# Kernel optimization log

Hardware: AMD Instinct MI355X
Metric: run time of the kernel (lower is better)

Reference implementation:

```python
import jax, jax.numpy as jnp
import numpy as np

N_EMBD = 1024
N_HEAD = 16
LATENT = 64
HEAD_DIM = N_EMBD // N_HEAD
B, T = 2, 2048
SCALE = 1.0 / np.sqrt(LATENT)


def setup_inputs() -> dict:
    key = jax.random.key(0)
    ks = jax.random.split(key, 10)
    s = lambda fan_in: 1.0 / np.sqrt(fan_in)
    return {
        "x": jax.random.normal(ks[0], (B, T, N_EMBD), dtype=jnp.float32),
        "Wq": jax.random.normal(ks[1], (N_EMBD, N_EMBD), dtype=jnp.float32) * s(N_EMBD),
        "bq": jnp.zeros((N_EMBD,), dtype=jnp.float32),
        "Wk": jax.random.normal(ks[2], (N_EMBD, N_HEAD * LATENT), dtype=jnp.float32) * s(N_EMBD),
        "bk": jnp.zeros((N_HEAD * LATENT,), dtype=jnp.float32),
        "Wv": jax.random.normal(ks[3], (N_EMBD, N_HEAD * LATENT), dtype=jnp.float32) * s(N_EMBD),
        "bv": jnp.zeros((N_HEAD * LATENT,), dtype=jnp.float32),
        "Wo": jax.random.normal(ks[4], (N_HEAD * LATENT, N_EMBD), dtype=jnp.float32) * s(N_HEAD * LATENT),
        "bo": jnp.zeros((N_EMBD,), dtype=jnp.float32),
        "Wc": jax.random.normal(ks[5], (HEAD_DIM, LATENT), dtype=jnp.float32) * s(HEAD_DIM),
    }


def reference(x, Wq, bq, Wk, bk, Wv, bv, Wo, bo, Wc):
    Bv, Tv, C = x.shape
    # projections
    q = (x @ Wq + bq).reshape(Bv, Tv, N_HEAD, HEAD_DIM)        # [B,T,H,Dh]
    k = (x @ Wk + bk).reshape(Bv, Tv, N_HEAD, LATENT)          # [B,T,H,L]
    v = (x @ Wv + bv).reshape(Bv, Tv, N_HEAD, LATENT)          # [B,T,H,L]
    # compress q into latent dim: [B,T,H,L]
    qc = jnp.einsum("bthd,dl->bthl", q, Wc)
    # attention scores [B,H,T,T]
    att = jnp.einsum("bthl,bshl->bhts", qc, k) * SCALE
    causal = jnp.tril(jnp.ones((Tv, Tv), dtype=bool))
    att = jnp.where(causal[None, None], att, -jnp.inf)
    att = jax.nn.softmax(att, axis=-1)
    y = jnp.einsum("bhts,bshl->bthl", att, v).reshape(Bv, Tv, N_HEAD * LATENT)
    return y @ Wo + bo
```

## Files before the change

kernel.cpp:

```cpp
#include <hip/hip_runtime.h>
#include <stdint.h>

#define TT 2048
#define BB 2
#define MROWS (BB*TT)
#define LSCALE 0.18033688011112043f

typedef unsigned short u16;
typedef __bf16 bf16x8 __attribute__((ext_vector_type(8)));
typedef float f32x4 __attribute__((ext_vector_type(4)));
typedef short s16x8 __attribute__((ext_vector_type(8)));
typedef unsigned short u16x4 __attribute__((ext_vector_type(4)));

#define GLOBAL_AS const __attribute__((address_space(1))) void*
#define LDS_AS __attribute__((address_space(3))) void*

__device__ __forceinline__ u16 f2b(float f){
  uint32_t u = __builtin_bit_cast(uint32_t, f);
  u = (u + 0x7FFFu + ((u >> 16) & 1u)) >> 16;
  return (u16)u;
}

__global__ __launch_bounds__(256) void prep(
    const float* __restrict__ x, const float* __restrict__ Wq,
    const float* __restrict__ Wc, const float* __restrict__ bq,
    const float* __restrict__ Wk, const float* __restrict__ Wv,
    const float* __restrict__ Wo,
    u16* __restrict__ xb, u16* __restrict__ WqcT, u16* __restrict__ WkT,
    u16* __restrict__ WvT, u16* __restrict__ WoT, float* __restrict__ bqc){
  const int i = blockIdx.x, t = threadIdx.x;
  if (i < 4096){
    int id = i * 256 + t;
    float4 v = ((const float4*)x)[id];
    u16x4 o; o.x = f2b(v.x); o.y = f2b(v.y); o.z = f2b(v.z); o.w = f2b(v.w);
    ((u16x4*)xb)[id] = o;
    return;
  }
  if (i < 7168){
    int j = i - 4096;
    int z = j >> 10, rem = j & 1023;
    const float* in = (z == 0) ? Wk : (z == 1) ? Wv : Wo;
    u16* out = (z == 0) ? WkT : (z == 1) ? WvT : WoT;
    __shared__ float tl[32][33];
    int tx = t & 31, ty = t >> 5;
    int c0 = (rem & 31) * 32, r0 = (rem >> 5) * 32;
    #pragma unroll
    for (int k = 0; k < 32; k += 8)
      tl[ty + k][tx] = in[(size_t)(r0 + ty + k) * 1024 + c0 + tx];
    __syncthreads();
    #pragma unroll
    for (int k = 0; k < 32; k += 8)
      out[(size_t)(c0 + ty + k) * 1024 + r0 + tx] = f2b(tl[tx][ty + k]);
    return;
  }
  __shared__ float wc[4096];
  #pragma unroll
  for (int k = 0; k < 16; ++k) wc[k * 256 + t] = Wc[k * 256 + t];
  __syncthreads();
  if (i == 7424){
    #pragma unroll
    for (int k = 0; k < 4; ++k){
      int nn = t * 4 + k;
      int h = nn >> 6, lc = nn & 63;
      float a = 0.f;
      #pragma unroll
      for (int dd = 0; dd < 64; ++dd) a += bq[h * 64 + dd] * wc[dd * 64 + lc];
      bqc[nn] = a;
    }
    return;
  }
  __shared__ float tile[64][65];
  const int j = i - 7168;
  const int db = j >> 4, hb = j & 15;
  {
    int dl = t >> 2, lq = t & 3;
    const float4* wq4 = (const float4*)(Wq + (size_t)(db * 64 + dl) * 1024 + hb * 64);
    float wqr[64];
    #pragma unroll
    for (int k = 0; k < 16; ++k){
      float4 v = wq4[k];
      wqr[k * 4] = v.x; wqr[k * 4 + 1] = v.y; wqr[k * 4 + 2] = v.z; wqr[k * 4 + 3] = v.w;
    }
    #pragma unroll
    for (int jj = 0; jj < 16; ++jj){
      int lc = lq * 16 + jj;
      float a = 0.f;
      #pragma unroll
      for (int dd = 0; dd < 64; ++dd) a += wqr[dd] * wc[dd * 64 + lc];
      tile[dl][lc] = a;
    }
  }
  __syncthreads();
  {
    int nl = t >> 2, dq = t & 3;
    u16* dst = WqcT + (size_t)(hb * 64 + nl) * 1024 + db * 64 + dq * 16;
    #pragma unroll
    for (int k = 0; k < 16; ++k)
      dst[k] = f2b(tile[dq * 16 + k][nl]);
  }
}

__global__ void transpose_v(const u16* __restrict__ vb, u16* __restrict__ vt){
  __shared__ u16 t[32][34];
  int tx = threadIdx.x & 31, ty = threadIdx.x >> 5;
  int s0 = blockIdx.x * 32, d0 = blockIdx.y * 32, bh = blockIdx.z;
  int b = bh >> 4, h = bh & 15;
  #pragma unroll
  for (int i = 0; i < 32; i += 8)
    t[ty + i][tx] = vb[(size_t)(b * TT + s0 + ty + i) * 1024 + h * 64 + d0 + tx];
  __syncthreads();
  #pragma unroll
  for (int i = 0; i < 32; i += 8)
    vt[((size_t)bh * 64 + d0 + ty + i) * TT + s0 + tx] = t[tx][ty + i];
}

__device__ __forceinline__ void gemm_tile(const u16* __restrict__ A, const u16* __restrict__ BT,
                                          int m0, int n0, int K, f32x4 (&acc)[4][4],
                                          u16* As, u16* Bs, int tid){
  const int wv = tid >> 6, l = tid & 63;
  const int aoff = ((wv >> 1) * 64 + (l & 15)) * 32 + ((l >> 4) << 3);
  const int boff = ((wv & 1) * 64 + (l & 15)) * 32 + ((l >> 4) << 3);
  const int ob0 = wv * 1024 + l * 16;
  for (int kt = 0; kt < K; kt += 32){
    __syncthreads();
    #pragma unroll
    for (int j = 0; j < 2; ++j){
      int ob = ob0 + j * 4096;
      int row = ob >> 6, col = (ob & 63) >> 1;
      __builtin_amdgcn_global_load_lds((GLOBAL_AS)(A + (size_t)(m0 + row) * 1024 + kt + col),
                                       (LDS_AS)(As + wv * 512 + j * 2048), 16, 0, 0);
      __builtin_amdgcn_global_load_lds((GLOBAL_AS)(BT + (size_t)(n0 + row) * 1024 + kt + col),
                                       (LDS_AS)(Bs + wv * 512 + j * 2048), 16, 0, 0);
    }
    __syncthreads();
    bf16x8 av[4], bw[4];
    #pragma unroll
    for (int m = 0; m < 4; ++m) av[m] = *(const bf16x8*)(As + aoff + m * 512);
    #pragma unroll
    for (int n = 0; n < 4; ++n) bw[n] = *(const bf16x8*)(Bs + boff + n * 512);
    #pragma unroll
    for (int m = 0; m < 4; ++m)
      #pragma unroll
      for (int n = 0; n < 4; ++n)
        acc[m][n] = __builtin_amdgcn_mfma_f32_16x16x32_bf16(av[m], bw[n], acc[m][n], 0, 0, 0);
  }
}

__global__ __launch_bounds__(256) void gemm_qkv(
    const u16* __restrict__ xb,
    const u16* __restrict__ W0T, const u16* __restrict__ W1T, const u16* __restrict__ W2T,
    const float* __restrict__ b0, const float* __restrict__ b1, const float* __restrict__ b2,
    u16* __restrict__ o0, u16* __restrict__ o1, u16* __restrict__ o2){
  __shared__ u16 As[4096], Bs[4096];
  const int z = blockIdx.z;
  const u16* BT = (z == 0) ? W0T : (z == 1) ? W1T : W2T;
  const float* bias = (z == 0) ? b0 : (z == 1) ? b1 : b2;
  u16* Out = (z == 0) ? o0 : (z == 1) ? o1 : o2;
  const float osc = (z == 0) ? LSCALE : 1.0f;
  const int n0 = blockIdx.x * 128, m0 = blockIdx.y * 128;
  const int tid = threadIdx.x, wv = tid >> 6, l = tid & 63;
  f32x4 acc[4][4] = {};
  gemm_tile(xb, BT, m0, n0, 1024, acc, As, Bs, tid);
  const int wr = wv >> 1, wc = wv & 1;
  #pragma unroll
  for (int n = 0; n < 4; ++n){
    int col = n0 + wc * 64 + n * 16 + (l & 15);
    float bb = bias[col];
    #pragma unroll
    for (int m = 0; m < 4; ++m){
      int r0 = m0 + wr * 64 + m * 16 + ((l >> 4) << 2);
      #pragma unroll
      for (int r = 0; r < 4; ++r)
        Out[(size_t)(r0 + r) * 1024 + col] = f2b((acc[m][n][r] + bb) * osc);
    }
  }
}

__global__ __launch_bounds__(256) void gemm_o(
    const u16* __restrict__ A, const u16* __restrict__ BT,
    const float* __restrict__ bias, float* __restrict__ Out){
  __shared__ u16 As[2048], Bs[4096];
  const int n0 = blockIdx.x * 128, m0 = blockIdx.y * 64;
  const int tid = threadIdx.x, wv = tid >> 6, l = tid & 63;
  const int wr = wv >> 1, wc = wv & 1;
  const int aoff = (wr * 32 + (l & 15)) * 32 + ((l >> 4) << 3);
  const int boff = (wc * 64 + (l & 15)) * 32 + ((l >> 4) << 3);
  const int obA = wv * 1024 + l * 16;
  const int rowA = obA >> 6, colA = (obA & 63) >> 1;
  const int ob0 = wv * 1024 + l * 16;
  f32x4 acc[2][4] = {};
  for (int kt = 0; kt < 1024; kt += 32){
    __syncthreads();
    __builtin_amdgcn_global_load_lds((GLOBAL_AS)(A + (size_t)(m0 + rowA) * 1024 + kt + colA),
                                     (LDS_AS)(As + wv * 512), 16, 0, 0);
    #pragma unroll
    for (int j = 0; j < 2; ++j){
      int ob = ob0 + j * 4096;
      int row = ob >> 6, col = (ob & 63) >> 1;
      __builtin_amdgcn_global_load_lds((GLOBAL_AS)(BT + (size_t)(n0 + row) * 1024 + kt + col),
                                       (LDS_AS)(Bs + wv * 512 + j * 2048), 16, 0, 0);
    }
    __syncthreads();
    bf16x8 av[2], bw[4];
    #pragma unroll
    for (int m = 0; m < 2; ++m) av[m] = *(const bf16x8*)(As + aoff + m * 512);
    #pragma unroll
    for (int n = 0; n < 4; ++n) bw[n] = *(const bf16x8*)(Bs + boff + n * 512);
    #pragma unroll
    for (int m = 0; m < 2; ++m)
      #pragma unroll
      for (int n = 0; n < 4; ++n)
        acc[m][n] = __builtin_amdgcn_mfma_f32_16x16x32_bf16(av[m], bw[n], acc[m][n], 0, 0, 0);
  }
  #pragma unroll
  for (int n = 0; n < 4; ++n){
    int col = n0 + wc * 64 + n * 16 + (l & 15);
    float bb = bias[col];
    #pragma unroll
    for (int m = 0; m < 2; ++m){
      int r0 = m0 + wr * 32 + m * 16 + ((l >> 4) << 2);
      #pragma unroll
      for (int r = 0; r < 4; ++r)
        Out[(size_t)(r0 + r) * 1024 + col] = acc[m][n][r] + bb;
    }
  }
}

__device__ const uint8_t qtab[32] = {
  31, 30, 29, 28, 27, 26, 25, 24,
   0,  1,  2,  3,  4,  5,  6,  7,
  23, 22, 21, 20, 19, 18, 17, 16,
   8,  9, 10, 11, 12, 13, 14, 15
};

__global__ __launch_bounds__(256) void attn(
    const u16* __restrict__ qcg, const u16* __restrict__ kg,
    const u16* __restrict__ vtg, u16* __restrict__ yg){
  __shared__ u16 Ks[4096], Vs[4096];
  __shared__ u16 Ps[4096];
  const int idx = blockIdx.x;
  const int qt = qtab[idx >> 5], bh = idx & 31;
  const int b = bh >> 4, h = bh & 15;
  const int q0 = qt * 64;
  const int tid = threadIdx.x, wv = tid >> 6, l = tid & 63;
  const int c4 = l >> 4, q16 = l & 15;
  const size_t base = (size_t)b * TT * 1024 + h * 64;
  const u16* Q = qcg + base;
  const u16* K = kg + base;
  const u16* Vt = vtg + (size_t)bh * 64 * TT;

  const int sr = tid >> 3;
  const int sc = (tid & 7) ^ (sr & 7);
  const u16* gK = K + (size_t)sr * 1024 + sc * 8;
  const u16* gV = Vt + (size_t)sr * TT + sc * 8;

  bf16x8 qf[2];
  {
    int qr = q0 + wv * 16 + q16;
    #pragma unroll
    for (int ks = 0; ks < 2; ++ks)
      qf[ks] = *(const bf16x8*)(Q + (size_t)qr * 1024 + ks * 32 + (c4 << 3));
  }
  bf16x8 ones;
  {
    s16x8 o1;
    #pragma unroll
    for (int j = 0; j < 8; ++j) o1[j] = (short)0x3F80;
    ones = __builtin_bit_cast(bf16x8, o1);
  }
  f32x4 yacc[4] = {};
  f32x4 sacc = {};
  float mrow = -1e30f;

  uint32_t* const PsW = (uint32_t*)Ps + wv * 512 + q16 * 32;
  const int pm = (q16 & 7) << 2;

  u16* const kd = Ks + wv * 512;
  u16* const vd = Vs + wv * 512;

  const int nt = qt + 1;
  for (int st = 0; st < nt; ++st){
    {
      const size_t o = (size_t)st * 64;
      __builtin_amdgcn_global_load_lds((GLOBAL_AS)(gK + o * 1024), (LDS_AS)kd, 16, 0, 0);
      __builtin_amdgcn_global_load_lds((GLOBAL_AS)(gK + (o + 32) * 1024), (LDS_AS)(kd + 2048), 16, 0, 0);
      __builtin_amdgcn_global_load_lds((GLOBAL_AS)(gV + o), (LDS_AS)vd, 16, 0, 0);
      __builtin_amdgcn_global_load_lds((GLOBAL_AS)(gV + o + 32 * TT), (LDS_AS)(vd + 2048), 16, 0, 0);
    }
    asm volatile("s_waitcnt vmcnt(0)" ::: "memory");
    __builtin_amdgcn_sched_barrier(0);
    __builtin_amdgcn_s_barrier();
    __builtin_amdgcn_sched_barrier(0);
    const int s0 = st * 64;
    f32x4 sf[4] = {};
    __builtin_amdgcn_s_setprio(1);
    #pragma unroll
    for (int ks = 0; ks < 2; ++ks)
      #pragma unroll
      for (int nf = 0; nf < 4; ++nf){
        int r = nf * 16 + q16, c = ks * 4 + c4;
        bf16x8 kf = *(const bf16x8*)(Ks + (r * 8 + (c ^ (r & 7))) * 8);
        sf[nf] = __builtin_amdgcn_mfma_f32_16x16x32_bf16(kf, qf[ks], sf[nf], 0, 0, 0);
      }
    __builtin_amdgcn_s_setprio(0);
    const int qa = q0 + wv * 16 + q16;
    float p[4][4];
    const bool domask = (st == qt);
    #pragma unroll
    for (int nf = 0; nf < 4; ++nf)
      #pragma unroll
      for (int r = 0; r < 4; ++r){
        float v_ = sf[nf][r];
        if (domask && (s0 + nf * 16 + c4 * 4 + r > qa)) v_ = -1e30f;
        p[nf][r] = v_;
      }
    float tmax = fmaxf(fmaxf(p[0][0], p[0][1]), p[0][2]);
    tmax = fmaxf(fmaxf(tmax, p[0][3]), p[1][0]);
    tmax = fmaxf(fmaxf(tmax, p[1][1]), p[1][2]);
    tmax = fmaxf(fmaxf(tmax, p[1][3]), p[2][0]);
    tmax = fmaxf(fmaxf(tmax, p[2][1]), p[2][2]);
    tmax = fmaxf(fmaxf(tmax, p[2][3]), p[3][0]);
    tmax = fmaxf(fmaxf(tmax, p[3][1]), p[3][2]);
    tmax = fmaxf(tmax, p[3][3]);
    tmax = fmaxf(tmax, __shfl_xor(tmax, 16));
    tmax = fmaxf(tmax, __shfl_xor(tmax, 32));
    if (__any(tmax > mrow + 8.0f)){
      float mnew = fmaxf(mrow, tmax);
      float resc = exp2f(mrow - mnew);
      sacc[0] *= resc;
      mrow = mnew;
      #pragma unroll
      for (int df = 0; df < 4; ++df)
        #pragma unroll
        for (int r = 0; r < 4; ++r) yacc[df][r] *= resc;
    }
    #pragma unroll
    for (int nf = 0; nf < 4; ++nf)
      #pragma unroll
      for (int r = 0; r < 4; ++r) p[nf][r] = exp2f(p[nf][r] - mrow);
    #pragma unroll
    for (int nf = 0; nf < 4; ++nf){
      uint32_t w0, w1;
      asm volatile("v_cvt_pk_bf16_f32 %0, %1, %2" : "=v"(w0) : "v"(p[nf][0]), "v"(p[nf][1]));
      asm volatile("v_cvt_pk_bf16_f32 %0, %1, %2" : "=v"(w1) : "v"(p[nf][2]), "v"(p[nf][3]));
      *(uint64_t*)(PsW + ((nf * 8 + c4 * 2) ^ pm)) = (uint64_t)w0 | ((uint64_t)w1 << 32);
    }
    asm volatile("s_waitcnt lgkmcnt(0)" ::: "memory");
    __builtin_amdgcn_sched_barrier(0);
    __builtin_amdgcn_s_setprio(1);
    #pragma unroll
    for (int ks2 = 0; ks2 < 2; ++ks2){
      bf16x8 pf = *(const bf16x8*)(PsW + ((ks2 * 16 + c4 * 4) ^ pm));
      sacc = __builtin_amdgcn_mfma_f32_16x16x32_bf16(ones, pf, sacc, 0, 0, 0);
      #pragma unroll
      for (int df = 0; df < 4; ++df){
        int rd = df * 16 + q16, cd = ks2 * 4 + c4;
        bf16x8 vf = *(const bf16x8*)(Vs + (rd * 8 + (cd ^ (rd & 7))) * 8);
        yacc[df] = __builtin_amdgcn_mfma_f32_16x16x32_bf16(vf, pf, yacc[df], 0, 0, 0);
      }
    }
    __builtin_amdgcn_s_setprio(0);
    __builtin_amdgcn_s_barrier();
  }

  const float inv = 1.f / sacc[0];
  const int qq = q0 + wv * 16 + q16;
  #pragma unroll
  for (int df = 0; df < 4; ++df){
    int d0 = df * 16 + c4 * 4;
    #pragma unroll
    for (int r = 0; r < 4; ++r)
      yg[(size_t)(b * TT + qq) * 1024 + h * 64 + d0 + r] = f2b(yacc[df][r] * inv);
  }
}

extern "C" void kernel_launch(void* const* d_in, const int* in_sizes, int n_in,
                              void* d_out, int out_size, void* d_ws, size_t ws_size,
                              hipStream_t stream){
  (void)in_sizes; (void)n_in; (void)out_size; (void)ws_size;
  const float* x  = (const float*)d_in[0];
  const float* Wq = (const float*)d_in[1];
  const float* bq = (const float*)d_in[2];
  const float* Wk = (const float*)d_in[3];
  const float* bk = (const float*)d_in[4];
  const float* Wv = (const float*)d_in[5];
  const float* bv = (const float*)d_in[6];
  const float* Wo = (const float*)d_in[7];
  const float* bo = (const float*)d_in[8];
  const float* Wc = (const float*)d_in[9];
  float* out = (float*)d_out;

  char* wsb = (char*)d_ws;
  u16* xb    = (u16*)(wsb);
  u16* yb    = (u16*)(wsb);
  u16* qcb   = (u16*)(wsb + (8u  << 20));
  u16* kb    = (u16*)(wsb + (16u << 20));
  u16* vb    = (u16*)(wsb + (24u << 20));
  u16* vtb   = (u16*)(wsb + (33u << 20));
  u16* WqcT  = (u16*)(wsb + (42u << 20));
  u16* WkT   = (u16*)(wsb + (44u << 20));
  u16* WvT   = (u16*)(wsb + (46u << 20));
  u16* WoT   = (u16*)(wsb + (48u << 20));
  float* bqc  = (float*)(wsb + (50u << 20));

  prep<<<7425, 256, 0, stream>>>(x, Wq, Wc, bq, Wk, Wv, Wo,
                                 xb, WqcT, WkT, WvT, WoT, bqc);
  gemm_qkv<<<dim3(8, 32, 3), 256, 0, stream>>>(xb, WqcT, WkT, WvT, bqc, bk, bv, qcb, kb, vb);
  transpose_v<<<dim3(64, 2, 32), 256, 0, stream>>>(vb, vtb);
  attn<<<dim3(1024), 256, 0, stream>>>(qcb, kb, vtb, yb);
  gemm_o<<<dim3(8, 64), 256, 0, stream>>>(yb, WoT, bo, out);
}
```

Before: 122.2 us.

## Process two key/value tiles per barrier in attention with peeled diagonal tile

The attention loop now loads two 64-key K/V tiles into double LDS buffers per iteration. It runs both QK MFMA groups, takes a joint row max with a single rescale check, then does the two PV updates. This halves the global-load waits, barriers and max/rescale reductions per key. The diagonal tile is peeled off so the causal mask only runs there, and an odd leftover tile gets its own handler. The cost is double the K/V LDS footprint, which may lower occupancy and raise register pressure from two score arrays.

```diff
diff --git a/kernel.cpp b/kernel.cpp
--- a/kernel.cpp
+++ b/kernel.cpp
@@ -236,7 +236,7 @@
 __global__ __launch_bounds__(256) void attn(
     const u16* __restrict__ qcg, const u16* __restrict__ kg,
     const u16* __restrict__ vtg, u16* __restrict__ yg){
-  __shared__ u16 Ks[4096], Vs[4096];
+  __shared__ u16 Ks[2][4096], Vs[2][4096];
   __shared__ u16 Ps[4096];
   const int idx = blockIdx.x;
   const int qt = qtab[idx >> 5], bh = idx & 31;
@@ -275,53 +275,26 @@
   uint32_t* const PsW = (uint32_t*)Ps + wv * 512 + q16 * 32;
   const int pm = (q16 & 7) << 2;
 
-  u16* const kd = Ks + wv * 512;
-  u16* const vd = Vs + wv * 512;
-
-  const int nt = qt + 1;
-  for (int st = 0; st < nt; ++st){
-    {
-      const size_t o = (size_t)st * 64;
-      __builtin_amdgcn_global_load_lds((GLOBAL_AS)(gK + o * 1024), (LDS_AS)kd, 16, 0, 0);
-      __builtin_amdgcn_global_load_lds((GLOBAL_AS)(gK + (o + 32) * 1024), (LDS_AS)(kd + 2048), 16, 0, 0);
-      __builtin_amdgcn_global_load_lds((GLOBAL_AS)(gV + o), (LDS_AS)vd, 16, 0, 0);
-      __builtin_amdgcn_global_load_lds((GLOBAL_AS)(gV + o + 32 * TT), (LDS_AS)(vd + 2048), 16, 0, 0);
-    }
-    asm volatile("s_waitcnt vmcnt(0)" ::: "memory");
-    __builtin_amdgcn_sched_barrier(0);
-    __builtin_amdgcn_s_barrier();
-    __builtin_amdgcn_sched_barrier(0);
-    const int s0 = st * 64;
-    f32x4 sf[4] = {};
-    __builtin_amdgcn_s_setprio(1);
+  auto stage = [&](int st, int buf){
+    const size_t o = (size_t)st * 64;
+    u16* kd = &Ks[buf][0] + wv * 512;
+    u16* vd = &Vs[buf][0] + wv * 512;
+    __builtin_amdgcn_global_load_lds((GLOBAL_AS)(gK + o * 1024), (LDS_AS)kd, 16, 0, 0);
+    __builtin_amdgcn_global_load_lds((GLOBAL_AS)(gK + (o + 32) * 1024), (LDS_AS)(kd + 2048), 16, 0, 0);
+    __builtin_amdgcn_global_load_lds((GLOBAL_AS)(gV + o), (LDS_AS)vd, 16, 0, 0);
+    __builtin_amdgcn_global_load_lds((GLOBAL_AS)(gV + o + 32 * TT), (LDS_AS)(vd + 2048), 16, 0, 0);
+  };
+  auto qkmm = [&](const u16* Kc, f32x4 (&sf)[4]){
     #pragma unroll
     for (int ks = 0; ks < 2; ++ks)
       #pragma unroll
       for (int nf = 0; nf < 4; ++nf){
         int r = nf * 16 + q16, c = ks * 4 + c4;
-        bf16x8 kf = *(const bf16x8*)(Ks + (r * 8 + (c ^ (r & 7))) * 8);
+        bf16x8 kf = *(const bf16x8*)(Kc + (r * 8 + (c ^ (r & 7))) * 8);
         sf[nf] = __builtin_amdgcn_mfma_f32_16x16x32_bf16(kf, qf[ks], sf[nf], 0, 0, 0);
       }
-    __builtin_amdgcn_s_setprio(0);
-    const int qa = q0 + wv * 16 + q16;
-    float p[4][4];
-    const bool domask = (st == qt);
-    #pragma unroll
-    for (int nf = 0; nf < 4; ++nf)
-      #pragma unroll
-      for (int r = 0; r < 4; ++r){
-        float v_ = sf[nf][r];
-        if (domask && (s0 + nf * 16 + c4 * 4 + r > qa)) v_ = -1e30f;
-        p[nf][r] = v_;
-      }
-    float tmax = fmaxf(fmaxf(p[0][0], p[0][1]), p[0][2]);
-    tmax = fmaxf(fmaxf(tmax, p[0][3]), p[1][0]);
-    tmax = fmaxf(fmaxf(tmax, p[1][1]), p[1][2]);
-    tmax = fmaxf(fmaxf(tmax, p[1][3]), p[2][0]);
-    tmax = fmaxf(fmaxf(tmax, p[2][1]), p[2][2]);
-    tmax = fmaxf(fmaxf(tmax, p[2][3]), p[3][0]);
-    tmax = fmaxf(fmaxf(tmax, p[3][1]), p[3][2]);
-    tmax = fmaxf(tmax, p[3][3]);
+  };
+  auto rescale = [&](float tmax){
     tmax = fmaxf(tmax, __shfl_xor(tmax, 16));
     tmax = fmaxf(tmax, __shfl_xor(tmax, 32));
     if (__any(tmax > mrow + 8.0f)){
@@ -334,15 +307,17 @@
         #pragma unroll
         for (int r = 0; r < 4; ++r) yacc[df][r] *= resc;
     }
+  };
+  auto halfstep = [&](f32x4 (&sf)[4], const u16* Vc){
     #pragma unroll
     for (int nf = 0; nf < 4; ++nf)
       #pragma unroll
-      for (int r = 0; r < 4; ++r) p[nf][r] = exp2f(p[nf][r] - mrow);
+      for (int r = 0; r < 4; ++r) sf[nf][r] = exp2f(sf[nf][r] - mrow);
     #pragma unroll
     for (int nf = 0; nf < 4; ++nf){
       uint32_t w0, w1;
-      asm volatile("v_cvt_pk_bf16_f32 %0, %1, %2" : "=v"(w0) : "v"(p[nf][0]), "v"(p[nf][1]));
-      asm volatile("v_cvt_pk_bf16_f32 %0, %1, %2" : "=v"(w1) : "v"(p[nf][2]), "v"(p[nf][3]));
+      asm volatile("v_cvt_pk_bf16_f32 %0, %1, %2" : "=v"(w0) : "v"(sf[nf][0]), "v"(sf[nf][1]));
+      asm volatile("v_cvt_pk_bf16_f32 %0, %1, %2" : "=v"(w1) : "v"(sf[nf][2]), "v"(sf[nf][3]));
       *(uint64_t*)(PsW + ((nf * 8 + c4 * 2) ^ pm)) = (uint64_t)w0 | ((uint64_t)w1 << 32);
     }
     asm volatile("s_waitcnt lgkmcnt(0)" ::: "memory");
@@ -355,12 +330,82 @@
       #pragma unroll
       for (int df = 0; df < 4; ++df){
         int rd = df * 16 + q16, cd = ks2 * 4 + c4;
-        bf16x8 vf = *(const bf16x8*)(Vs + (rd * 8 + (cd ^ (rd & 7))) * 8);
+        bf16x8 vf = *(const bf16x8*)(Vc + (rd * 8 + (cd ^ (rd & 7))) * 8);
         yacc[df] = __builtin_amdgcn_mfma_f32_16x16x32_bf16(vf, pf, yacc[df], 0, 0, 0);
       }
     }
     __builtin_amdgcn_s_setprio(0);
+  };
+
+  const int npair = qt >> 1;
+  for (int pp = 0; pp < npair; ++pp){
+    stage(2 * pp, 0);
+    stage(2 * pp + 1, 1);
+    asm volatile("s_waitcnt vmcnt(0)" ::: "memory");
+    __builtin_amdgcn_sched_barrier(0);
     __builtin_amdgcn_s_barrier();
+    __builtin_amdgcn_sched_barrier(0);
+    f32x4 sf0[4] = {}, sf1[4] = {};
+    __builtin_amdgcn_s_setprio(1);
+    qkmm(&Ks[0][0], sf0);
+    qkmm(&Ks[1][0], sf1);
+    __builtin_amdgcn_s_setprio(0);
+    float tmax = sf0[0][0];
+    #pragma unroll
+    for (int nf = 0; nf < 4; ++nf)
+      #pragma unroll
+      for (int r = 0; r < 4; ++r){
+        tmax = fmaxf(tmax, sf0[nf][r]);
+        tmax = fmaxf(tmax, sf1[nf][r]);
+      }
+    rescale(tmax);
+    halfstep(sf0, &Vs[0][0]);
+    halfstep(sf1, &Vs[1][0]);
+    __builtin_amdgcn_s_barrier();
+  }
+  if (qt & 1){
+    stage(qt - 1, 0);
+    asm volatile("s_waitcnt vmcnt(0)" ::: "memory");
+    __builtin_amdgcn_sched_barrier(0);
+    __builtin_amdgcn_s_barrier();
+    __builtin_amdgcn_sched_barrier(0);
+    f32x4 sf0[4] = {};
+    __builtin_amdgcn_s_setprio(1);
+    qkmm(&Ks[0][0], sf0);
+    __builtin_amdgcn_s_setprio(0);
+    float tmax = sf0[0][0];
+    #pragma unroll
+    for (int nf = 0; nf < 4; ++nf)
+      #pragma unroll
+      for (int r = 0; r < 4; ++r) tmax = fmaxf(tmax, sf0[nf][r]);
+    rescale(tmax);
+    halfstep(sf0, &Vs[0][0]);
+    __builtin_amdgcn_s_barrier();
+  }
+  {
+    const int s0 = qt * 64;
+    stage(qt, 0);
+    asm volatile("s_waitcnt vmcnt(0)" ::: "memory");
+    __builtin_amdgcn_sched_barrier(0);
+    __builtin_amdgcn_s_barrier();
+    __builtin_amdgcn_sched_barrier(0);
+    f32x4 sf0[4] = {};
+    __builtin_amdgcn_s_setprio(1);
+    qkmm(&Ks[0][0], sf0);
+    __builtin_amdgcn_s_setprio(0);
+    const int qa = q0 + wv * 16 + q16;
+    #pragma unroll
+    for (int nf = 0; nf < 4; ++nf)
+      #pragma unroll
+      for (int r = 0; r < 4; ++r)
+        if (s0 + nf * 16 + c4 * 4 + r > qa) sf0[nf][r] = -1e30f;
+    float tmax = sf0[0][0];
+    #pragma unroll
+    for (int nf = 0; nf < 4; ++nf)
+      #pragma unroll
+      for (int r = 0; r < 4; ++r) tmax = fmaxf(tmax, sf0[nf][r]);
+    rescale(tmax);
+    halfstep(sf0, &Vs[0][0]);
   }
 
   const float inv = 1.f / sacc[0];
```

Measured after the change: 130.4 us. +6.8%, slower.
